# Optimization experiments

Hardware: AMD Instinct MI355X
Metric: run time of the kernel (lower is better)

## Reference

```python
import jax, jax.numpy as jnp
import numpy as np

B, S, D, H = 2, 2048, 1024, 16
HD = D // H  # head_dim = 64


def setup_inputs() -> dict:
    key = jax.random.key(0)
    ks = jax.random.split(key, 10)
    sc = 1.0 / np.sqrt(D)
    x = jax.random.normal(ks[0], (B, S, D), dtype=jnp.float32)
    # causal mask, 0 = masked (module does masked_fill(mask == 0, -1e9))
    mask = jnp.broadcast_to(jnp.tril(jnp.ones((S, S), dtype=jnp.int32)), (B, S, S))
    return {
        "x": x,
        "mask": mask,
        "Wq": jax.random.normal(ks[1], (D, D), dtype=jnp.float32) * sc,
        "bq": jnp.zeros((D,), dtype=jnp.float32),
        "Wk": jax.random.normal(ks[2], (D, D), dtype=jnp.float32) * sc,
        "bk": jnp.zeros((D,), dtype=jnp.float32),
        "Wv": jax.random.normal(ks[3], (D, D), dtype=jnp.float32) * sc,
        "bv": jnp.zeros((D,), dtype=jnp.float32),
        "Wo": jax.random.normal(ks[4], (D, D), dtype=jnp.float32) * sc,
        "bo": jnp.zeros((D,), dtype=jnp.float32),
    }


def reference(x, mask, Wq, bq, Wk, bk, Wv, bv, Wo, bo):
    b, s, _ = x.shape
    # torch nn.Linear: y = x @ W.T + b
    def split_heads(t):
        return t.reshape(b, s, H, HD).transpose(0, 2, 1, 3)  # [B,H,S,hd]
    q = split_heads(x @ Wq.T + bq)
    k = split_heads(x @ Wk.T + bk)
    v = split_heads(x @ Wv.T + bv)
    scores = jnp.einsum("bhqd,bhkd->bhqk", q, k) / jnp.sqrt(jnp.float32(HD))
    scores = jnp.where(mask[:, None, :, :] == 0, jnp.float32(-1e9), scores)
    w = jax.nn.softmax(scores, axis=-1)
    out = jnp.einsum("bhqk,bhkd->bhqd", w, v)  # [B,H,S,hd]
    out = out.transpose(0, 2, 1, 3).reshape(b, s, D)
    return out @ Wo.T + bo
```

## Files before the change

kernel.cpp:

```cpp
#include <hip/hip_runtime.h>
#include <cstdint>


typedef __bf16 bf16x8 __attribute__((ext_vector_type(8)));
typedef float f32x4 __attribute__((ext_vector_type(4)));

__device__ inline f32x4 mfma16(bf16x8 a, bf16x8 b, f32x4 c) {
    return __builtin_amdgcn_mfma_f32_16x16x32_bf16(a, b, c, 0, 0, 0);
}

__device__ inline uint16_t f2bf(float f) {
    uint32_t u = __builtin_bit_cast(uint32_t, f);
    u += 0x7FFFu + ((u >> 16) & 1u);
    return (uint16_t)(u >> 16);
}

__device__ inline void gload_lds16(const uint16_t* g, uint16_t* l) {
    __builtin_amdgcn_global_load_lds(
        (const __attribute__((address_space(1))) uint32_t*)g,
        (__attribute__((address_space(3))) uint32_t*)l, 16, 0, 0);
}

__global__ __launch_bounds__(256) void cast_all(const float* __restrict__ x,
                                                const float* __restrict__ wq,
                                                const float* __restrict__ wk,
                                                const float* __restrict__ wv,
                                                const float* __restrict__ wo,
                                                uint16_t* __restrict__ xbf,
                                                uint16_t* __restrict__ wbf) {
    int i = blockIdx.x * 256 + threadIdx.x;
    float4 v;
    uint64_t* dp;
    if (i < (1 << 20)) {
        v = ((const float4*)x)[i];
        dp = (uint64_t*)xbf + i;
    } else {
        int j = i - (1 << 20);
        const float* ws[4] = {wq, wk, wv, wo};
        v = ((const float4*)ws[j >> 18])[j & 0x3FFFF];
        dp = (uint64_t*)wbf + j;
    }
    uint64_t p = (uint64_t)f2bf(v.x) | ((uint64_t)f2bf(v.y) << 16) |
                 ((uint64_t)f2bf(v.z) << 32) | ((uint64_t)f2bf(v.w) << 48);
    *dp = p;
}

template<int OUTF32, int BN>
__global__ __launch_bounds__(256) void gemm128(const uint16_t* __restrict__ A,
                                               const uint16_t* __restrict__ W,
                                               const float* __restrict__ b0,
                                               const float* __restrict__ b1,
                                               const float* __restrict__ b2,
                                               void* __restrict__ o0,
                                               void* __restrict__ o1,
                                               void* __restrict__ o2,
                                               int K, float s0, float s1, float s2) {
    constexpr int NT = BN / 32;
    __shared__ __align__(16) uint16_t SH[2][(128 + BN) * 32];
    const int tid = threadIdx.x;
    const int lane = tid & 63, w = tid >> 6;
    const int l16 = lane & 15, quad = lane >> 4;
    const int wm = w & 1, wn = w >> 1;
    const int m0 = blockIdx.x * 128, n0 = blockIdx.y * BN;

    f32x4 acc[4][NT] = {};

    const int ci0 = w * 128 + lane;
    const uint16_t* ga0 = A + (size_t)(m0 + (ci0 >> 2)) * K + (ci0 & 3) * 8;
    const int ci1 = ci0 + 64;
    const uint16_t* ga1 = A + (size_t)(m0 + (ci1 >> 2)) * K + (ci1 & 3) * 8;
    const uint16_t* gb0 = W + (size_t)(n0 + (ci0 >> 2)) * K + (ci0 & 3) * 8;
    const uint16_t* gb1 = W + (size_t)(n0 + (ci1 >> 2)) * K + (ci1 & 3) * 8;
    const uint16_t* gbS = W + (size_t)(n0 + (tid >> 2)) * K + (tid & 3) * 8;

    uint16_t* A0 = SH[0];
    uint16_t* B0 = SH[0] + 128 * 32;
    uint16_t* A1 = SH[1];
    uint16_t* B1 = SH[1] + 128 * 32;

    gload_lds16(ga0, A0 + (w * 2 + 0) * 512);
    gload_lds16(ga1, A0 + (w * 2 + 1) * 512);
    if constexpr (BN == 128) {
        gload_lds16(gb0, B0 + (w * 2 + 0) * 512);
        gload_lds16(gb1, B0 + (w * 2 + 1) * 512);
    } else {
        gload_lds16(gbS, B0 + w * 512);
    }

    const int niter = K >> 5;
    for (int i = 0; i < niter; ++i) {
        __syncthreads();
        if (i + 1 < niter) {
            const int k1 = (i + 1) << 5;
            uint16_t* Ad = (i & 1) ? A0 : A1;
            uint16_t* Bd = (i & 1) ? B0 : B1;
            gload_lds16(ga0 + k1, Ad + (w * 2 + 0) * 512);
            gload_lds16(ga1 + k1, Ad + (w * 2 + 1) * 512);
            if constexpr (BN == 128) {
                gload_lds16(gb0 + k1, Bd + (w * 2 + 0) * 512);
                gload_lds16(gb1 + k1, Bd + (w * 2 + 1) * 512);
            } else {
                gload_lds16(gbS + k1, Bd + w * 512);
            }
        }
        const uint16_t* Ab = (i & 1) ? A1 : A0;
        const uint16_t* Bb = (i & 1) ? B1 : B0;
        bf16x8 af[4], bw[NT];
#pragma unroll
        for (int t = 0; t < 4; ++t)
            af[t] = *(const bf16x8*)(Ab + (wm * 64 + t * 16 + l16) * 32 + quad * 8);
#pragma unroll
        for (int t = 0; t < NT; ++t)
            bw[t] = *(const bf16x8*)(Bb + (wn * (BN / 2) + t * 16 + l16) * 32 + quad * 8);
#pragma unroll
        for (int mt = 0; mt < 4; ++mt)
#pragma unroll
            for (int nt = 0; nt < NT; ++nt)
                acc[mt][nt] = mfma16(af[mt], bw[nt], acc[mt][nt]);
    }

    const int seg = n0 >> 10, lc0 = n0 & 1023;
    const float* bp = (seg == 0) ? b0 : (seg == 1 ? b1 : b2);
    const float scale = (seg == 0) ? s0 : (seg == 1 ? s1 : s2);
    void* op = (seg == 0) ? o0 : (seg == 1 ? o1 : o2);

    if constexpr (OUTF32) {
#pragma unroll
        for (int nt = 0; nt < NT; ++nt) {
            int lcol = lc0 + wn * (BN / 2) + nt * 16 + l16;
            float bc = bp[lcol];
#pragma unroll
            for (int mt = 0; mt < 4; ++mt)
#pragma unroll
                for (int r = 0; r < 4; ++r) {
                    int row = m0 + wm * 64 + mt * 16 + quad * 4 + r;
                    ((float*)op)[(size_t)row * 1024 + lcol] = (acc[mt][nt][r] + bc) * scale;
                }
        }
    } else {
        __syncthreads();
        uint16_t* EP = &SH[0][0];
#pragma unroll
        for (int nt = 0; nt < NT; ++nt) {
            float bc = bp[lc0 + wn * (BN / 2) + nt * 16 + l16];
#pragma unroll
            for (int mt = 0; mt < 4; ++mt)
#pragma unroll
                for (int r = 0; r < 4; ++r)
                    EP[(wm * 64 + mt * 16 + quad * 4 + r) * 128 +
                       wn * (BN / 2) + nt * 16 + l16] =
                        f2bf((acc[mt][nt][r] + bc) * scale);
        }
        __syncthreads();
#pragma unroll
        for (int p = 0; p < 8; ++p) {
            int row = p * 16 + (tid >> 4);
            int c8 = (tid & 15) * 8;
            uint4 v = *(const uint4*)(EP + row * 128 + c8);
            *(uint4*)((uint16_t*)op + (size_t)(m0 + row) * 1024 + lc0 + c8) = v;
        }
    }
}

__global__ __launch_bounds__(256) void transpose_v(const uint16_t* __restrict__ V,
                                                   uint16_t* __restrict__ Vt) {
    __shared__ __align__(16) uint16_t T[64 * 72];
    const int s0 = blockIdx.x * 64;
    const int bh = blockIdx.y;
    const int b = bh >> 4, h = bh & 15;
    const int tid = threadIdx.x;
    const int r = tid >> 2, c = tid & 3;
#pragma unroll
    for (int half = 0; half < 2; ++half) {
        uint4 v = *(const uint4*)(V + (size_t)(b * 2048 + s0 + r) * 1024 + h * 64 + half * 32 + c * 8);
        *(uint4*)(T + r * 72 + half * 32 + c * 8) = v;
    }
    __syncthreads();
#pragma unroll
    for (int it = 0; it < 2; ++it) {
        int id = it * 256 + tid;
        int d = id >> 3, c8 = (id & 7) * 8;
        uint32_t wpk[4];
#pragma unroll
        for (int jj = 0; jj < 4; ++jj) {
            uint32_t lo = T[(c8 + 2 * jj) * 72 + d];
            uint32_t hi = T[(c8 + 2 * jj + 1) * 72 + d];
            wpk[jj] = lo | (hi << 16);
        }
        uint4 o; o.x = wpk[0]; o.y = wpk[1]; o.z = wpk[2]; o.w = wpk[3];
        *(uint4*)(Vt + ((size_t)bh * 64 + d) * 2048 + s0 + c8) = o;
    }
}

__global__ __launch_bounds__(256) void attn_kernel(const uint16_t* __restrict__ Q,
                                                   const uint16_t* __restrict__ K,
                                                   const uint16_t* __restrict__ Vt,
                                                   uint16_t* __restrict__ att) {
    const int S = 2048, D = 1024;
    __shared__ __align__(16) uint16_t Klds[2][64 * 72];
    __shared__ __align__(16) uint16_t Vlds[2][64 * 72];
    __shared__ __align__(16) uint16_t Plds[4 * 32 * 72];

    const int bh = blockIdx.y;
    const int qb = (bh & 16) ? (int)blockIdx.x : 15 - (int)blockIdx.x;
    const int niter = 2 * qb + 2, kb_diag = 2 * qb;

    const int b = bh >> 4, h = bh & 15;
    const int tid = threadIdx.x, lane = tid & 63, w = tid >> 6;
    const int l16 = lane & 15, quad = lane >> 4;
    const int q0 = qb * 128;
    const size_t baseQK = (size_t)b * S * D + h * 64;
    uint16_t* Pw = Plds + w * (32 * 72);

    bf16x8 aq[2][2];
#pragma unroll
    for (int mt = 0; mt < 2; ++mt)
#pragma unroll
        for (int c = 0; c < 2; ++c)
            aq[mt][c] = *(const bf16x8*)(Q + baseQK +
                (size_t)(q0 + w * 32 + mt * 16 + l16) * D + c * 32 + quad * 8);

    bf16x8 ones;
#pragma unroll
    for (int j = 0; j < 8; ++j) ones[j] = (__bf16)1.0f;

    f32x4 accO[2][4] = {};
    f32x4 accL[2] = {};

    const int srow = tid >> 2, scq = tid & 3;
    const uint16_t* Kg = K + baseQK + (size_t)srow * D + scq * 16;
    const uint16_t* Vg = Vt + ((size_t)bh * 64 + srow) * S + scq * 16;
    const int soff = srow * 72 + scq * 16;

    uint4 kA, kB, vA, vB;
    kA = *(const uint4*)Kg; kB = *(const uint4*)(Kg + 8);
    vA = *(const uint4*)Vg; vB = *(const uint4*)(Vg + 8);
    *(uint4*)(Klds[0] + soff)     = kA;
    *(uint4*)(Klds[0] + soff + 8) = kB;
    *(uint4*)(Vlds[0] + soff)     = vA;
    *(uint4*)(Vlds[0] + soff + 8) = vB;
    {
        const uint16_t* kg = Kg + (size_t)64 * D;
        const uint16_t* vg = Vg + 64;
        kA = *(const uint4*)kg; kB = *(const uint4*)(kg + 8);
        vA = *(const uint4*)vg; vB = *(const uint4*)(vg + 8);
    }
    __syncthreads();

    for (int kb = 0; kb < niter; ++kb) {
        const uint16_t* Kb = Klds[kb & 1];
        const uint16_t* Vb = Vlds[kb & 1];

        if (kb + 1 < niter) {
            uint16_t* Kd = (uint16_t*)Klds[(kb + 1) & 1];
            uint16_t* Vd = (uint16_t*)Vlds[(kb + 1) & 1];
            *(uint4*)(Kd + soff)     = kA;
            *(uint4*)(Kd + soff + 8) = kB;
            *(uint4*)(Vd + soff)     = vA;
            *(uint4*)(Vd + soff + 8) = vB;
            if (kb + 2 < niter) {
                const uint16_t* kg = Kg + (size_t)((kb + 2) * 64) * D;
                const uint16_t* vg = Vg + (kb + 2) * 64;
                kA = *(const uint4*)kg; kB = *(const uint4*)(kg + 8);
                vA = *(const uint4*)vg; vB = *(const uint4*)(vg + 8);
            }
        }

        f32x4 sc[2][4];
#pragma unroll
        for (int t = 0; t < 4; ++t) {
            bf16x8 bk0 = *(const bf16x8*)(Kb + (t * 16 + l16) * 72 + quad * 8);
            bf16x8 bk1 = *(const bf16x8*)(Kb + (t * 16 + l16) * 72 + 32 + quad * 8);
            f32x4 z0 = {}; f32x4 z1 = {};
            sc[0][t] = mfma16(aq[0][1], bk1, mfma16(aq[0][0], bk0, z0));
            sc[1][t] = mfma16(aq[1][1], bk1, mfma16(aq[1][0], bk0, z1));
        }

        bf16x8 bv0[4], bv1[4];
#pragma unroll
        for (int nt = 0; nt < 4; ++nt) {
            bv0[nt] = *(const bf16x8*)(Vb + (nt * 16 + l16) * 72 + quad * 8);
            bv1[nt] = *(const bf16x8*)(Vb + (nt * 16 + l16) * 72 + 32 + quad * 8);
        }

        if (kb < kb_diag) {
#pragma unroll
            for (int mt = 0; mt < 2; ++mt)
#pragma unroll
                for (int r = 0; r < 4; ++r)
#pragma unroll
                    for (int t = 0; t < 4; ++t) {
                        float p = __builtin_amdgcn_exp2f(sc[mt][t][r]);
                        Pw[(mt * 16 + quad * 4 + r) * 72 + t * 16 + l16] =
                            (uint16_t)(__builtin_bit_cast(uint32_t, p) >> 16);
                    }
        } else {
#pragma unroll
            for (int mt = 0; mt < 2; ++mt)
#pragma unroll
                for (int r = 0; r < 4; ++r) {
                    const int qrow = q0 + w * 32 + mt * 16 + quad * 4 + r;
#pragma unroll
                    for (int t = 0; t < 4; ++t) {
                        float s = sc[mt][t][r];
                        int kcol = kb * 64 + t * 16 + l16;
                        if (kcol > qrow) s = -1e30f;
                        float p = __builtin_amdgcn_exp2f(s);
                        Pw[(mt * 16 + quad * 4 + r) * 72 + t * 16 + l16] =
                            (uint16_t)(__builtin_bit_cast(uint32_t, p) >> 16);
                    }
                }
        }

        __asm__ volatile("s_waitcnt lgkmcnt(0)" ::: "memory");

        bf16x8 ap0[2], ap1[2];
#pragma unroll
        for (int mt = 0; mt < 2; ++mt) {
            ap0[mt] = *(const bf16x8*)(Pw + (mt * 16 + l16) * 72 + quad * 8);
            ap1[mt] = *(const bf16x8*)(Pw + (mt * 16 + l16) * 72 + 32 + quad * 8);
        }
#pragma unroll
        for (int nt = 0; nt < 4; ++nt) {
            accO[0][nt] = mfma16(ap1[0], bv1[nt], mfma16(ap0[0], bv0[nt], accO[0][nt]));
            accO[1][nt] = mfma16(ap1[1], bv1[nt], mfma16(ap0[1], bv0[nt], accO[1][nt]));
        }
        accL[0] = mfma16(ap1[0], ones, mfma16(ap0[0], ones, accL[0]));
        accL[1] = mfma16(ap1[1], ones, mfma16(ap0[1], ones, accL[1]));

        if (kb + 1 < niter) __syncthreads();
    }

    __asm__ volatile("s_waitcnt lgkmcnt(0)" ::: "memory");
#pragma unroll
    for (int mt = 0; mt < 2; ++mt)
#pragma unroll
        for (int r = 0; r < 4; ++r) {
            float inv = __builtin_amdgcn_rcpf(accL[mt][r]);
            const int rl = mt * 16 + quad * 4 + r;
#pragma unroll
            for (int nt = 0; nt < 4; ++nt)
                Pw[rl * 72 + nt * 16 + l16] = f2bf(accO[mt][nt][r] * inv);
        }
    __asm__ volatile("s_waitcnt lgkmcnt(0)" ::: "memory");
#pragma unroll
    for (int p = 0; p < 4; ++p) {
        int row = p * 8 + (lane >> 3);
        int c8 = (lane & 7) * 8;
        uint4 v = *(const uint4*)(Pw + row * 72 + c8);
        *(uint4*)(att + (size_t)(b * S + q0 + w * 32 + row) * 1024 + h * 64 + c8) = v;
    }
}

extern "C" void kernel_launch(void* const* d_in, const int* in_sizes, int n_in,
                              void* d_out, int out_size, void* d_ws, size_t ws_size,
                              hipStream_t stream) {
    const float* x  = (const float*)d_in[0];
    const float* Wq = (const float*)d_in[2];
    const float* bq = (const float*)d_in[3];
    const float* Wk = (const float*)d_in[4];
    const float* bk = (const float*)d_in[5];
    const float* Wv = (const float*)d_in[6];
    const float* bv = (const float*)d_in[7];
    const float* Wo = (const float*)d_in[8];
    const float* bo = (const float*)d_in[9];
    float* out = (float*)d_out;

    const int B = 2, S = 2048, D = 1024, H = 16;
    const int M = B * S;

    uint8_t* w = (uint8_t*)d_ws;
    uint16_t* xbf  = (uint16_t*)(w);
    uint16_t* wqbf = (uint16_t*)(w + (size_t)( 8 << 20));
    uint16_t* qbf  = (uint16_t*)(w + (size_t)(16 << 20));
    uint16_t* kbf  = (uint16_t*)(w + (size_t)(24 << 20));
    uint16_t* vbf  = (uint16_t*)(w + (size_t)(32 << 20));
    uint16_t* vtbf = (uint16_t*)(w + (size_t)(40 << 20));
    uint16_t* wobf = wqbf + (size_t)3 * D * D;
    uint16_t* attbf = xbf;

    cast_all<<<dim3((1 << 21) / 256), dim3(256), 0, stream>>>(
        x, Wq, Wk, Wv, Wo, xbf, wqbf);

    gemm128<0, 128><<<dim3(M / 128, 3072 / 128), dim3(256), 0, stream>>>(
        xbf, wqbf, bq, bk, bv, qbf, kbf, vbf, D, 0.125f * 1.44269504f, 1.0f, 1.0f);

    transpose_v<<<dim3(S / 64, B * H), dim3(256), 0, stream>>>(vbf, vtbf);

    attn_kernel<<<dim3(16, B * H), dim3(256), 0, stream>>>(qbf, kbf, vtbf, attbf);

    gemm128<1, 64><<<dim3(M / 128, 1024 / 64), dim3(256), 0, stream>>>(
        attbf, wobf, bo, bo, bo, out, out, out, D, 1.0f, 1.0f, 1.0f);
}
```

Baseline: 197.9 us.

## Fuse V transpose into QKV GEMM epilogue and use 8-wave attention blocks

```diff
diff --git a/kernel.cpp b/kernel.cpp
--- a/kernel.cpp
+++ b/kernel.cpp
@@ -56,7 +56,7 @@
                                                void* __restrict__ o2,
                                                int K, float s0, float s1, float s2) {
     constexpr int NT = BN / 32;
-    __shared__ __align__(16) uint16_t SH[2][(128 + BN) * 32];
+    __shared__ __align__(16) uint16_t SH[2 * (128 + BN) * 32];
     const int tid = threadIdx.x;
     const int lane = tid & 63, w = tid >> 6;
     const int l16 = lane & 15, quad = lane >> 4;
@@ -73,10 +73,10 @@
     const uint16_t* gb1 = W + (size_t)(n0 + (ci1 >> 2)) * K + (ci1 & 3) * 8;
     const uint16_t* gbS = W + (size_t)(n0 + (tid >> 2)) * K + (tid & 3) * 8;
 
-    uint16_t* A0 = SH[0];
-    uint16_t* B0 = SH[0] + 128 * 32;
-    uint16_t* A1 = SH[1];
-    uint16_t* B1 = SH[1] + 128 * 32;
+    uint16_t* A0 = SH;
+    uint16_t* B0 = SH + 128 * 32;
+    uint16_t* A1 = SH + (128 + BN) * 32;
+    uint16_t* B1 = A1 + 128 * 32;
 
     gload_lds16(ga0, A0 + (w * 2 + 0) * 512);
     gload_lds16(ga1, A0 + (w * 2 + 1) * 512);
@@ -139,7 +139,7 @@
         }
     } else {
         __syncthreads();
-        uint16_t* EP = &SH[0][0];
+        uint16_t* EP = SH;
 #pragma unroll
         for (int nt = 0; nt < NT; ++nt) {
             float bc = bp[lc0 + wn * (BN / 2) + nt * 16 + l16];
@@ -152,54 +152,45 @@
                         f2bf((acc[mt][nt][r] + bc) * scale);
         }
         __syncthreads();
-#pragma unroll
-        for (int p = 0; p < 8; ++p) {
-            int row = p * 16 + (tid >> 4);
-            int c8 = (tid & 15) * 8;
-            uint4 v = *(const uint4*)(EP + row * 128 + c8);
-            *(uint4*)((uint16_t*)op + (size_t)(m0 + row) * 1024 + lc0 + c8) = v;
-        }
-    }
-}
-
-__global__ __launch_bounds__(256) void transpose_v(const uint16_t* __restrict__ V,
-                                                   uint16_t* __restrict__ Vt) {
-    __shared__ __align__(16) uint16_t T[64 * 72];
-    const int s0 = blockIdx.x * 64;
-    const int bh = blockIdx.y;
-    const int b = bh >> 4, h = bh & 15;
-    const int tid = threadIdx.x;
-    const int r = tid >> 2, c = tid & 3;
-#pragma unroll
-    for (int half = 0; half < 2; ++half) {
-        uint4 v = *(const uint4*)(V + (size_t)(b * 2048 + s0 + r) * 1024 + h * 64 + half * 32 + c * 8);
-        *(uint4*)(T + r * 72 + half * 32 + c * 8) = v;
-    }
-    __syncthreads();
-#pragma unroll
-    for (int it = 0; it < 2; ++it) {
-        int id = it * 256 + tid;
-        int d = id >> 3, c8 = (id & 7) * 8;
-        uint32_t wpk[4];
-#pragma unroll
-        for (int jj = 0; jj < 4; ++jj) {
-            uint32_t lo = T[(c8 + 2 * jj) * 72 + d];
-            uint32_t hi = T[(c8 + 2 * jj + 1) * 72 + d];
-            wpk[jj] = lo | (hi << 16);
-        }
-        uint4 o; o.x = wpk[0]; o.y = wpk[1]; o.z = wpk[2]; o.w = wpk[3];
-        *(uint4*)(Vt + ((size_t)bh * 64 + d) * 2048 + s0 + c8) = o;
-    }
-}
-
-__global__ __launch_bounds__(256) void attn_kernel(const uint16_t* __restrict__ Q,
+        if (seg == 2) {
+            const int bb = m0 >> 11, s0v = m0 & 2047;
+            const int h0 = (n0 - 2048) >> 6;
+            uint16_t* vtb = (uint16_t*)op + ((size_t)(bb * 16 + h0) * 64) * 2048 + s0v;
+#pragma unroll
+            for (int it = 0; it < 8; ++it) {
+                int id = it * 256 + tid;
+                int c = id & 127, sg = id >> 7;
+                uint32_t wpk[4];
+#pragma unroll
+                for (int jj = 0; jj < 4; ++jj) {
+                    uint32_t lo = EP[(sg * 8 + 2 * jj) * 128 + c];
+                    uint32_t hi = EP[(sg * 8 + 2 * jj + 1) * 128 + c];
+                    wpk[jj] = lo | (hi << 16);
+                }
+                uint4 o; o.x = wpk[0]; o.y = wpk[1]; o.z = wpk[2]; o.w = wpk[3];
+                *(uint4*)(vtb + (size_t)c * 2048 + sg * 8) = o;
+            }
+        } else {
+#pragma unroll
+            for (int p = 0; p < 8; ++p) {
+                int row = p * 16 + (tid >> 4);
+                int c8 = (tid & 15) * 8;
+                uint4 v = *(const uint4*)(EP + row * 128 + c8);
+                *(uint4*)((uint16_t*)op + (size_t)(m0 + row) * 1024 + lc0 + c8) = v;
+            }
+        }
+    }
+}
+
+__global__ __launch_bounds__(512) void attn_kernel(const uint16_t* __restrict__ Q,
                                                    const uint16_t* __restrict__ K,
                                                    const uint16_t* __restrict__ Vt,
                                                    uint16_t* __restrict__ att) {
     const int S = 2048, D = 1024;
-    __shared__ __align__(16) uint16_t Klds[2][64 * 72];
-    __shared__ __align__(16) uint16_t Vlds[2][64 * 72];
-    __shared__ __align__(16) uint16_t Plds[4 * 32 * 72];
+    constexpr int LD = 72;
+    __shared__ __align__(16) uint16_t Klds[2][64 * LD];
+    __shared__ __align__(16) uint16_t Vlds[2][64 * LD];
+    __shared__ __align__(16) uint16_t Plds[8 * 16 * LD];
 
     const int bh = blockIdx.y;
     const int qb = (bh & 16) ? (int)blockIdx.x : 15 - (int)blockIdx.x;
@@ -210,40 +201,34 @@
     const int l16 = lane & 15, quad = lane >> 4;
     const int q0 = qb * 128;
     const size_t baseQK = (size_t)b * S * D + h * 64;
-    uint16_t* Pw = Plds + w * (32 * 72);
-
-    bf16x8 aq[2][2];
-#pragma unroll
-    for (int mt = 0; mt < 2; ++mt)
-#pragma unroll
-        for (int c = 0; c < 2; ++c)
-            aq[mt][c] = *(const bf16x8*)(Q + baseQK +
-                (size_t)(q0 + w * 32 + mt * 16 + l16) * D + c * 32 + quad * 8);
+    uint16_t* Pw = Plds + w * (16 * LD);
+
+    bf16x8 aq[2];
+#pragma unroll
+    for (int c = 0; c < 2; ++c)
+        aq[c] = *(const bf16x8*)(Q + baseQK +
+            (size_t)(q0 + w * 16 + l16) * D + c * 32 + quad * 8);
 
     bf16x8 ones;
 #pragma unroll
     for (int j = 0; j < 8; ++j) ones[j] = (__bf16)1.0f;
 
-    f32x4 accO[2][4] = {};
-    f32x4 accL[2] = {};
-
-    const int srow = tid >> 2, scq = tid & 3;
-    const uint16_t* Kg = K + baseQK + (size_t)srow * D + scq * 16;
-    const uint16_t* Vg = Vt + ((size_t)bh * 64 + srow) * S + scq * 16;
-    const int soff = srow * 72 + scq * 16;
-
-    uint4 kA, kB, vA, vB;
-    kA = *(const uint4*)Kg; kB = *(const uint4*)(Kg + 8);
-    vA = *(const uint4*)Vg; vB = *(const uint4*)(Vg + 8);
-    *(uint4*)(Klds[0] + soff)     = kA;
-    *(uint4*)(Klds[0] + soff + 8) = kB;
-    *(uint4*)(Vlds[0] + soff)     = vA;
-    *(uint4*)(Vlds[0] + soff + 8) = vB;
+    f32x4 accO[4] = {};
+    f32x4 accL = {};
+
+    const int srow = tid >> 3, scq = tid & 7;
+    const uint16_t* Kg = K + baseQK + (size_t)srow * D + scq * 8;
+    const uint16_t* Vg = Vt + ((size_t)bh * 64 + srow) * S + scq * 8;
+    const int soff = srow * LD + scq * 8;
+
+    uint4 kA, vA;
+    kA = *(const uint4*)Kg;
+    vA = *(const uint4*)Vg;
+    *(uint4*)(Klds[0] + soff) = kA;
+    *(uint4*)(Vlds[0] + soff) = vA;
     {
-        const uint16_t* kg = Kg + (size_t)64 * D;
-        const uint16_t* vg = Vg + 64;
-        kA = *(const uint4*)kg; kB = *(const uint4*)(kg + 8);
-        vA = *(const uint4*)vg; vB = *(const uint4*)(vg + 8);
+        kA = *(const uint4*)(Kg + (size_t)64 * D);
+        vA = *(const uint4*)(Vg + 64);
     }
     __syncthreads();
 
@@ -252,103 +237,83 @@
         const uint16_t* Vb = Vlds[kb & 1];
 
         if (kb + 1 < niter) {
-            uint16_t* Kd = (uint16_t*)Klds[(kb + 1) & 1];
-            uint16_t* Vd = (uint16_t*)Vlds[(kb + 1) & 1];
-            *(uint4*)(Kd + soff)     = kA;
-            *(uint4*)(Kd + soff + 8) = kB;
-            *(uint4*)(Vd + soff)     = vA;
-            *(uint4*)(Vd + soff + 8) = vB;
+            *(uint4*)((uint16_t*)Klds[(kb + 1) & 1] + soff) = kA;
+            *(uint4*)((uint16_t*)Vlds[(kb + 1) & 1] + soff) = vA;
             if (kb + 2 < niter) {
-                const uint16_t* kg = Kg + (size_t)((kb + 2) * 64) * D;
-                const uint16_t* vg = Vg + (kb + 2) * 64;
-                kA = *(const uint4*)kg; kB = *(const uint4*)(kg + 8);
-                vA = *(const uint4*)vg; vB = *(const uint4*)(vg + 8);
-            }
-        }
-
-        f32x4 sc[2][4];
+                kA = *(const uint4*)(Kg + (size_t)((kb + 2) * 64) * D);
+                vA = *(const uint4*)(Vg + (kb + 2) * 64);
+            }
+        }
+
+        f32x4 sc[4];
 #pragma unroll
         for (int t = 0; t < 4; ++t) {
-            bf16x8 bk0 = *(const bf16x8*)(Kb + (t * 16 + l16) * 72 + quad * 8);
-            bf16x8 bk1 = *(const bf16x8*)(Kb + (t * 16 + l16) * 72 + 32 + quad * 8);
-            f32x4 z0 = {}; f32x4 z1 = {};
-            sc[0][t] = mfma16(aq[0][1], bk1, mfma16(aq[0][0], bk0, z0));
-            sc[1][t] = mfma16(aq[1][1], bk1, mfma16(aq[1][0], bk0, z1));
+            bf16x8 bk0 = *(const bf16x8*)(Kb + (t * 16 + l16) * LD + quad * 8);
+            bf16x8 bk1 = *(const bf16x8*)(Kb + (t * 16 + l16) * LD + 32 + quad * 8);
+            f32x4 z = {};
+            sc[t] = mfma16(aq[1], bk1, mfma16(aq[0], bk0, z));
         }
 
         bf16x8 bv0[4], bv1[4];
 #pragma unroll
         for (int nt = 0; nt < 4; ++nt) {
-            bv0[nt] = *(const bf16x8*)(Vb + (nt * 16 + l16) * 72 + quad * 8);
-            bv1[nt] = *(const bf16x8*)(Vb + (nt * 16 + l16) * 72 + 32 + quad * 8);
+            bv0[nt] = *(const bf16x8*)(Vb + (nt * 16 + l16) * LD + quad * 8);
+            bv1[nt] = *(const bf16x8*)(Vb + (nt * 16 + l16) * LD + 32 + quad * 8);
         }
 
         if (kb < kb_diag) {
 #pragma unroll
-            for (int mt = 0; mt < 2; ++mt)
-#pragma unroll
-                for (int r = 0; r < 4; ++r)
-#pragma unroll
-                    for (int t = 0; t < 4; ++t) {
-                        float p = __builtin_amdgcn_exp2f(sc[mt][t][r]);
-                        Pw[(mt * 16 + quad * 4 + r) * 72 + t * 16 + l16] =
-                            (uint16_t)(__builtin_bit_cast(uint32_t, p) >> 16);
-                    }
+            for (int r = 0; r < 4; ++r)
+#pragma unroll
+                for (int t = 0; t < 4; ++t) {
+                    float p = __builtin_amdgcn_exp2f(sc[t][r]);
+                    Pw[(quad * 4 + r) * LD + t * 16 + l16] =
+                        (uint16_t)(__builtin_bit_cast(uint32_t, p) >> 16);
+                }
         } else {
 #pragma unroll
-            for (int mt = 0; mt < 2; ++mt)
-#pragma unroll
-                for (int r = 0; r < 4; ++r) {
-                    const int qrow = q0 + w * 32 + mt * 16 + quad * 4 + r;
-#pragma unroll
-                    for (int t = 0; t < 4; ++t) {
-                        float s = sc[mt][t][r];
-                        int kcol = kb * 64 + t * 16 + l16;
-                        if (kcol > qrow) s = -1e30f;
-                        float p = __builtin_amdgcn_exp2f(s);
-                        Pw[(mt * 16 + quad * 4 + r) * 72 + t * 16 + l16] =
-                            (uint16_t)(__builtin_bit_cast(uint32_t, p) >> 16);
-                    }
+            for (int r = 0; r < 4; ++r) {
+                const int qrow = q0 + w * 16 + quad * 4 + r;
+#pragma unroll
+                for (int t = 0; t < 4; ++t) {
+                    float s = sc[t][r];
+                    int kcol = kb * 64 + t * 16 + l16;
+                    if (kcol > qrow) s = -1e30f;
+                    float p = __builtin_amdgcn_exp2f(s);
+                    Pw[(quad * 4 + r) * LD + t * 16 + l16] =
+                        (uint16_t)(__builtin_bit_cast(uint32_t, p) >> 16);
                 }
+            }
         }
 
         __asm__ volatile("s_waitcnt lgkmcnt(0)" ::: "memory");
 
-        bf16x8 ap0[2], ap1[2];
-#pragma unroll
-        for (int mt = 0; mt < 2; ++mt) {
-            ap0[mt] = *(const bf16x8*)(Pw + (mt * 16 + l16) * 72 + quad * 8);
-            ap1[mt] = *(const bf16x8*)(Pw + (mt * 16 + l16) * 72 + 32 + quad * 8);
-        }
-#pragma unroll
-        for (int nt = 0; nt < 4; ++nt) {
-            accO[0][nt] = mfma16(ap1[0], bv1[nt], mfma16(ap0[0], bv0[nt], accO[0][nt]));
-            accO[1][nt] = mfma16(ap1[1], bv1[nt], mfma16(ap0[1], bv0[nt], accO[1][nt]));
-        }
-        accL[0] = mfma16(ap1[0], ones, mfma16(ap0[0], ones, accL[0]));
-        accL[1] = mfma16(ap1[1], ones, mfma16(ap0[1], ones, accL[1]));
+        bf16x8 ap0 = *(const bf16x8*)(Pw + l16 * LD + quad * 8);
+        bf16x8 ap1 = *(const bf16x8*)(Pw + l16 * LD + 32 + quad * 8);
+#pragma unroll
+        for (int nt = 0; nt < 4; ++nt)
+            accO[nt] = mfma16(ap1, bv1[nt], mfma16(ap0, bv0[nt], accO[nt]));
+        accL = mfma16(ap1, ones, mfma16(ap0, ones, accL));
 
         if (kb + 1 < niter) __syncthreads();
     }
 
     __asm__ volatile("s_waitcnt lgkmcnt(0)" ::: "memory");
 #pragma unroll
-    for (int mt = 0; mt < 2; ++mt)
-#pragma unroll
-        for (int r = 0; r < 4; ++r) {
-            float inv = __builtin_amdgcn_rcpf(accL[mt][r]);
-            const int rl = mt * 16 + quad * 4 + r;
-#pragma unroll
-            for (int nt = 0; nt < 4; ++nt)
-                Pw[rl * 72 + nt * 16 + l16] = f2bf(accO[mt][nt][r] * inv);
-        }
+    for (int r = 0; r < 4; ++r) {
+        float inv = __builtin_amdgcn_rcpf(accL[r]);
+        const int rl = quad * 4 + r;
+#pragma unroll
+        for (int nt = 0; nt < 4; ++nt)
+            Pw[rl * LD + nt * 16 + l16] = f2bf(accO[nt][r] * inv);
+    }
     __asm__ volatile("s_waitcnt lgkmcnt(0)" ::: "memory");
 #pragma unroll
-    for (int p = 0; p < 4; ++p) {
+    for (int p = 0; p < 2; ++p) {
         int row = p * 8 + (lane >> 3);
         int c8 = (lane & 7) * 8;
-        uint4 v = *(const uint4*)(Pw + row * 72 + c8);
-        *(uint4*)(att + (size_t)(b * S + q0 + w * 32 + row) * 1024 + h * 64 + c8) = v;
+        uint4 v = *(const uint4*)(Pw + row * LD + c8);
+        *(uint4*)(att + (size_t)(b * S + q0 + w * 16 + row) * 1024 + h * 64 + c8) = v;
     }
 }
 
@@ -374,7 +339,6 @@
     uint16_t* wqbf = (uint16_t*)(w + (size_t)( 8 << 20));
     uint16_t* qbf  = (uint16_t*)(w + (size_t)(16 << 20));
     uint16_t* kbf  = (uint16_t*)(w + (size_t)(24 << 20));
-    uint16_t* vbf  = (uint16_t*)(w + (size_t)(32 << 20));
     uint16_t* vtbf = (uint16_t*)(w + (size_t)(40 << 20));
     uint16_t* wobf = wqbf + (size_t)3 * D * D;
     uint16_t* attbf = xbf;
@@ -383,11 +347,9 @@
         x, Wq, Wk, Wv, Wo, xbf, wqbf);
 
     gemm128<0, 128><<<dim3(M / 128, 3072 / 128), dim3(256), 0, stream>>>(
-        xbf, wqbf, bq, bk, bv, qbf, kbf, vbf, D, 0.125f * 1.44269504f, 1.0f, 1.0f);
-
-    transpose_v<<<dim3(S / 64, B * H), dim3(256), 0, stream>>>(vbf, vtbf);
-
-    attn_kernel<<<dim3(16, B * H), dim3(256), 0, stream>>>(qbf, kbf, vtbf, attbf);
+        xbf, wqbf, bq, bk, bv, qbf, kbf, vtbf, D, 0.125f * 1.44269504f, 1.0f, 1.0f);
+
+    attn_kernel<<<dim3(16, B * H), dim3(512), 0, stream>>>(qbf, kbf, vtbf, attbf);
 
     gemm128<1, 64><<<dim3(M / 128, 1024 / 64), dim3(256), 0, stream>>>(
         attbf, wobf, bo, bo, bo, out, out, out, D, 1.0f, 1.0f, 1.0f);
```

Result: no change. 197.5 us (-0.2%).

## Fuse V transpose into QKV GEMM epilogue and swizzle P tile in LDS

Applied to the files above, without the earlier changes.

```diff
diff --git a/kernel.cpp b/kernel.cpp
--- a/kernel.cpp
+++ b/kernel.cpp
@@ -56,7 +56,7 @@
                                                void* __restrict__ o2,
                                                int K, float s0, float s1, float s2) {
     constexpr int NT = BN / 32;
-    __shared__ __align__(16) uint16_t SH[2][(128 + BN) * 32];
+    __shared__ __align__(16) uint16_t SH[2 * (128 + BN) * 32];
     const int tid = threadIdx.x;
     const int lane = tid & 63, w = tid >> 6;
     const int l16 = lane & 15, quad = lane >> 4;
@@ -73,10 +73,10 @@
     const uint16_t* gb1 = W + (size_t)(n0 + (ci1 >> 2)) * K + (ci1 & 3) * 8;
     const uint16_t* gbS = W + (size_t)(n0 + (tid >> 2)) * K + (tid & 3) * 8;
 
-    uint16_t* A0 = SH[0];
-    uint16_t* B0 = SH[0] + 128 * 32;
-    uint16_t* A1 = SH[1];
-    uint16_t* B1 = SH[1] + 128 * 32;
+    uint16_t* A0 = SH;
+    uint16_t* B0 = SH + 128 * 32;
+    uint16_t* A1 = SH + (128 + BN) * 32;
+    uint16_t* B1 = A1 + 128 * 32;
 
     gload_lds16(ga0, A0 + (w * 2 + 0) * 512);
     gload_lds16(ga1, A0 + (w * 2 + 1) * 512);
@@ -139,7 +139,7 @@
         }
     } else {
         __syncthreads();
-        uint16_t* EP = &SH[0][0];
+        uint16_t* EP = SH;
 #pragma unroll
         for (int nt = 0; nt < NT; ++nt) {
             float bc = bp[lc0 + wn * (BN / 2) + nt * 16 + l16];
@@ -152,43 +152,33 @@
                         f2bf((acc[mt][nt][r] + bc) * scale);
         }
         __syncthreads();
-#pragma unroll
-        for (int p = 0; p < 8; ++p) {
-            int row = p * 16 + (tid >> 4);
-            int c8 = (tid & 15) * 8;
-            uint4 v = *(const uint4*)(EP + row * 128 + c8);
-            *(uint4*)((uint16_t*)op + (size_t)(m0 + row) * 1024 + lc0 + c8) = v;
-        }
-    }
-}
-
-__global__ __launch_bounds__(256) void transpose_v(const uint16_t* __restrict__ V,
-                                                   uint16_t* __restrict__ Vt) {
-    __shared__ __align__(16) uint16_t T[64 * 72];
-    const int s0 = blockIdx.x * 64;
-    const int bh = blockIdx.y;
-    const int b = bh >> 4, h = bh & 15;
-    const int tid = threadIdx.x;
-    const int r = tid >> 2, c = tid & 3;
-#pragma unroll
-    for (int half = 0; half < 2; ++half) {
-        uint4 v = *(const uint4*)(V + (size_t)(b * 2048 + s0 + r) * 1024 + h * 64 + half * 32 + c * 8);
-        *(uint4*)(T + r * 72 + half * 32 + c * 8) = v;
-    }
-    __syncthreads();
-#pragma unroll
-    for (int it = 0; it < 2; ++it) {
-        int id = it * 256 + tid;
-        int d = id >> 3, c8 = (id & 7) * 8;
-        uint32_t wpk[4];
-#pragma unroll
-        for (int jj = 0; jj < 4; ++jj) {
-            uint32_t lo = T[(c8 + 2 * jj) * 72 + d];
-            uint32_t hi = T[(c8 + 2 * jj + 1) * 72 + d];
-            wpk[jj] = lo | (hi << 16);
-        }
-        uint4 o; o.x = wpk[0]; o.y = wpk[1]; o.z = wpk[2]; o.w = wpk[3];
-        *(uint4*)(Vt + ((size_t)bh * 64 + d) * 2048 + s0 + c8) = o;
+        if (seg == 2) {
+            const int bb = m0 >> 11, s0v = m0 & 2047;
+            const int h0 = (n0 - 2048) >> 6;
+            uint16_t* vtb = (uint16_t*)op + ((size_t)(bb * 16 + h0) * 64) * 2048 + s0v;
+#pragma unroll
+            for (int it = 0; it < 8; ++it) {
+                int id = it * 256 + tid;
+                int c = id & 127, sg = id >> 7;
+                uint32_t wpk[4];
+#pragma unroll
+                for (int jj = 0; jj < 4; ++jj) {
+                    uint32_t lo = EP[(sg * 8 + 2 * jj) * 128 + c];
+                    uint32_t hi = EP[(sg * 8 + 2 * jj + 1) * 128 + c];
+                    wpk[jj] = lo | (hi << 16);
+                }
+                uint4 o; o.x = wpk[0]; o.y = wpk[1]; o.z = wpk[2]; o.w = wpk[3];
+                *(uint4*)(vtb + (size_t)c * 2048 + sg * 8) = o;
+            }
+        } else {
+#pragma unroll
+            for (int p = 0; p < 8; ++p) {
+                int row = p * 16 + (tid >> 4);
+                int c8 = (tid & 15) * 8;
+                uint4 v = *(const uint4*)(EP + row * 128 + c8);
+                *(uint4*)((uint16_t*)op + (size_t)(m0 + row) * 1024 + lc0 + c8) = v;
+            }
+        }
     }
 }
 
@@ -197,9 +187,10 @@
                                                    const uint16_t* __restrict__ Vt,
                                                    uint16_t* __restrict__ att) {
     const int S = 2048, D = 1024;
-    __shared__ __align__(16) uint16_t Klds[2][64 * 72];
-    __shared__ __align__(16) uint16_t Vlds[2][64 * 72];
-    __shared__ __align__(16) uint16_t Plds[4 * 32 * 72];
+    constexpr int LD = 72;
+    __shared__ __align__(16) uint16_t Klds[2][64 * LD];
+    __shared__ __align__(16) uint16_t Vlds[2][64 * LD];
+    __shared__ __align__(16) uint16_t Plds[4 * 32 * LD];
 
     const int bh = blockIdx.y;
     const int qb = (bh & 16) ? (int)blockIdx.x : 15 - (int)blockIdx.x;
@@ -210,7 +201,9 @@
     const int l16 = lane & 15, quad = lane >> 4;
     const int q0 = qb * 128;
     const size_t baseQK = (size_t)b * S * D + h * 64;
-    uint16_t* Pw = Plds + w * (32 * 72);
+    uint16_t* Pw = Plds + w * (32 * LD);
+    const int qh = quad >> 1;
+    const int rx = ((l16 >> 3) & 1) << 4;
 
     bf16x8 aq[2][2];
 #pragma unroll
@@ -230,7 +223,7 @@
     const int srow = tid >> 2, scq = tid & 3;
     const uint16_t* Kg = K + baseQK + (size_t)srow * D + scq * 16;
     const uint16_t* Vg = Vt + ((size_t)bh * 64 + srow) * S + scq * 16;
-    const int soff = srow * 72 + scq * 16;
+    const int soff = srow * LD + scq * 16;
 
     uint4 kA, kB, vA, vB;
     kA = *(const uint4*)Kg; kB = *(const uint4*)(Kg + 8);
@@ -269,8 +262,8 @@
         f32x4 sc[2][4];
 #pragma unroll
         for (int t = 0; t < 4; ++t) {
-            bf16x8 bk0 = *(const bf16x8*)(Kb + (t * 16 + l16) * 72 + quad * 8);
-            bf16x8 bk1 = *(const bf16x8*)(Kb + (t * 16 + l16) * 72 + 32 + quad * 8);
+            bf16x8 bk0 = *(const bf16x8*)(Kb + (t * 16 + l16) * LD + quad * 8);
+            bf16x8 bk1 = *(const bf16x8*)(Kb + (t * 16 + l16) * LD + 32 + quad * 8);
             f32x4 z0 = {}; f32x4 z1 = {};
             sc[0][t] = mfma16(aq[0][1], bk1, mfma16(aq[0][0], bk0, z0));
             sc[1][t] = mfma16(aq[1][1], bk1, mfma16(aq[1][0], bk0, z1));
@@ -279,8 +272,8 @@
         bf16x8 bv0[4], bv1[4];
 #pragma unroll
         for (int nt = 0; nt < 4; ++nt) {
-            bv0[nt] = *(const bf16x8*)(Vb + (nt * 16 + l16) * 72 + quad * 8);
-            bv1[nt] = *(const bf16x8*)(Vb + (nt * 16 + l16) * 72 + 32 + quad * 8);
+            bv0[nt] = *(const bf16x8*)(Vb + (nt * 16 + l16) * LD + quad * 8);
+            bv1[nt] = *(const bf16x8*)(Vb + (nt * 16 + l16) * LD + 32 + quad * 8);
         }
 
         if (kb < kb_diag) {
@@ -291,7 +284,7 @@
 #pragma unroll
                     for (int t = 0; t < 4; ++t) {
                         float p = __builtin_amdgcn_exp2f(sc[mt][t][r]);
-                        Pw[(mt * 16 + quad * 4 + r) * 72 + t * 16 + l16] =
+                        Pw[(mt * 16 + quad * 4 + r) * LD + (t ^ qh) * 16 + l16] =
                             (uint16_t)(__builtin_bit_cast(uint32_t, p) >> 16);
                     }
         } else {
@@ -306,7 +299,7 @@
                         int kcol = kb * 64 + t * 16 + l16;
                         if (kcol > qrow) s = -1e30f;
                         float p = __builtin_amdgcn_exp2f(s);
-                        Pw[(mt * 16 + quad * 4 + r) * 72 + t * 16 + l16] =
+                        Pw[(mt * 16 + quad * 4 + r) * LD + (t ^ qh) * 16 + l16] =
                             (uint16_t)(__builtin_bit_cast(uint32_t, p) >> 16);
                     }
                 }
@@ -317,8 +310,8 @@
         bf16x8 ap0[2], ap1[2];
 #pragma unroll
         for (int mt = 0; mt < 2; ++mt) {
-            ap0[mt] = *(const bf16x8*)(Pw + (mt * 16 + l16) * 72 + quad * 8);
-            ap1[mt] = *(const bf16x8*)(Pw + (mt * 16 + l16) * 72 + 32 + quad * 8);
+            ap0[mt] = *(const bf16x8*)(Pw + (mt * 16 + l16) * LD + ((quad * 8) ^ rx));
+            ap1[mt] = *(const bf16x8*)(Pw + (mt * 16 + l16) * LD + ((32 + quad * 8) ^ rx));
         }
 #pragma unroll
         for (int nt = 0; nt < 4; ++nt) {
@@ -340,14 +333,14 @@
             const int rl = mt * 16 + quad * 4 + r;
 #pragma unroll
             for (int nt = 0; nt < 4; ++nt)
-                Pw[rl * 72 + nt * 16 + l16] = f2bf(accO[mt][nt][r] * inv);
+                Pw[rl * LD + nt * 16 + l16] = f2bf(accO[mt][nt][r] * inv);
         }
     __asm__ volatile("s_waitcnt lgkmcnt(0)" ::: "memory");
 #pragma unroll
     for (int p = 0; p < 4; ++p) {
         int row = p * 8 + (lane >> 3);
         int c8 = (lane & 7) * 8;
-        uint4 v = *(const uint4*)(Pw + row * 72 + c8);
+        uint4 v = *(const uint4*)(Pw + row * LD + c8);
         *(uint4*)(att + (size_t)(b * S + q0 + w * 32 + row) * 1024 + h * 64 + c8) = v;
     }
 }
@@ -374,7 +367,6 @@
     uint16_t* wqbf = (uint16_t*)(w + (size_t)( 8 << 20));
     uint16_t* qbf  = (uint16_t*)(w + (size_t)(16 << 20));
     uint16_t* kbf  = (uint16_t*)(w + (size_t)(24 << 20));
-    uint16_t* vbf  = (uint16_t*)(w + (size_t)(32 << 20));
     uint16_t* vtbf = (uint16_t*)(w + (size_t)(40 << 20));
     uint16_t* wobf = wqbf + (size_t)3 * D * D;
     uint16_t* attbf = xbf;
@@ -383,9 +375,7 @@
         x, Wq, Wk, Wv, Wo, xbf, wqbf);
 
     gemm128<0, 128><<<dim3(M / 128, 3072 / 128), dim3(256), 0, stream>>>(
-        xbf, wqbf, bq, bk, bv, qbf, kbf, vbf, D, 0.125f * 1.44269504f, 1.0f, 1.0f);
-
-    transpose_v<<<dim3(S / 64, B * H), dim3(256), 0, stream>>>(vbf, vtbf);
+        xbf, wqbf, bq, bk, bv, qbf, kbf, vtbf, D, 0.125f * 1.44269504f, 1.0f, 1.0f);
 
     attn_kernel<<<dim3(16, B * H), dim3(256), 0, stream>>>(qbf, kbf, vtbf, attbf);
 
```

After: 196.1 us. No clear change (-0.9%).
